# Kernel tuning notes

Measured on AMD Instinct MI355X. Metric: run time of the kernel, lower is better.

## Reference

```python
import jax, jax.numpy as jnp
import numpy as np

SIGMA = 300.0      # args.sigma (temporal gaussian kernel width, frames)
DECAY = 0.9        # args.memory_decay; avg() uses weight = 1/decay per older entry
W_TIME = 1.0       # args.temporal_weight
ORIG_LOSS = 1.0    # args.originalloss_weight
EPS = 1e-7         # BCE clamp


def _get_msg(bank_values, bank_times, bank_mask, ids, times, future):
    """Vectorized MessagePassing.get_msg: per-(id,time) gather of stored
    messages, temporal-kernel + decay weighted average. Mirrors avg():
    out = sum_i dw_i * kernel_i * v_i / sum_i dw_i, dw_i = (1/decay)^rank_i
    with rank over entries passing the past/future condition, zeros if empty."""
    vals = bank_values[ids]                      # [N, M, C]
    ts = bank_times[ids].astype(jnp.float32)     # [N, M]
    mk = bank_mask[ids]                          # [N, M]
    t0 = times.astype(jnp.float32)[:, None]      # [N, 1]
    cond = (ts > t0) if future else (ts < t0)
    m = (mk & cond).astype(vals.dtype)           # [N, M]
    kern = jnp.exp(-((ts - t0) ** 2) / (2.0 * SIGMA ** 2))
    rank = jnp.cumsum(m, axis=1) - m             # exclusive rank among valid entries
    dw = ((1.0 / DECAY) ** rank) * m             # decay weights, masked
    num = jnp.einsum('nm,nmc->nc', dw * kern, vals)
    den = jnp.sum(dw, axis=1, keepdims=True)     # denominator excludes kernel (as avg())
    msg = jnp.where(den > 0, num / jnp.maximum(den, EPS), 0.0)
    return msg * W_TIME


def _bce(p, t):
    p = jnp.clip(p, EPS, 1.0 - EPS)
    return -jnp.mean(t * jnp.log(p) + (1.0 - t) * jnp.log(1.0 - p))


def setup_inputs() -> dict:
    key = jax.random.key(0)
    k = jax.random.split(key, 8)
    N, C, NUM_IDS, M = 512, 157, 10000, 20
    return {
        'a': jax.random.normal(k[0], (N, C), jnp.float32),
        'aa': jax.random.normal(k[1], (N, C, C), jnp.float32),
        'target': jax.random.uniform(k[2], (N, C), jnp.float32),
        'bank_values': jax.random.uniform(k[3], (NUM_IDS, M, C), jnp.float32),
        'bank_times': jax.random.randint(k[4], (NUM_IDS, M), 0, 1000, jnp.int32),
        'bank_mask': jnp.ones((NUM_IDS, M), dtype=bool),
        'ids': jax.random.randint(k[5], (N,), 0, NUM_IDS, jnp.int32),
        'times': jax.random.randint(k[6], (N,), 0, 1000, jnp.int32),
    }


def reference(a, aa, target, bank_values, bank_times, bank_mask, ids, times):
    # msg/fmsg come from stored (detached) data in the original
    msg = jax.lax.stop_gradient(_get_msg(bank_values, bank_times, bank_mask, ids, times, future=False))
    fmsg = jax.lax.stop_gradient(_get_msg(bank_values, bank_times, bank_mask, ids, times, future=True))
    # qa = a + sum_i aa[n,i,j]*msg[n,i] + sum_j aa[n,i,j]*fmsg[n,j]
    qa = a + jnp.einsum('nij,ni->nj', aa, msg) + jnp.einsum('nij,nj->ni', aa, fmsg)
    qa = jax.nn.sigmoid(qa)
    loss = _bce(qa, target) + _bce(jax.nn.sigmoid(a), target) * ORIG_LOSS
    # training, adjustment=False: pastloss = futureloss = 0
    loss = loss / 3.0
    return qa, loss
```

## Files before the change

### kernel.cpp

```cpp
#include <hip/hip_runtime.h>
#include <math.h>

#define N 512
#define C 157
#define M 20

__device__ __forceinline__ float sigmoidf_(float x) {
    return 1.0f / (1.0f + __expf(-x));
}
__device__ __forceinline__ float ntload(const float* p) {
    return __builtin_nontemporal_load(p);
}

__global__ __launch_bounds__(256) void atf_main_kernel(
    const float* __restrict__ a,
    const float* __restrict__ aa,
    const float* __restrict__ target,
    const float* __restrict__ bank_values,
    const int* __restrict__ bank_times,
    const int* __restrict__ bank_mask,
    const int* __restrict__ ids,
    const int* __restrict__ times,
    float* __restrict__ out,
    float* __restrict__ loss_part)
{
    const int n    = blockIdx.x;
    const int tid  = threadIdx.x;
    const int wave = tid >> 6;
    const int lane = tid & 63;

    __shared__ float s_ts[M];
    __shared__ int   s_mk[M];
    __shared__ float s_msg[C];
    __shared__ float s_fmsg[C];
    __shared__ float s_row[C];
    __shared__ float s_colp[4][C];
    __shared__ float s_red[4];

    const int   id = ids[n];
    const float t0 = (float)times[n];

    if (tid < M) {
        s_ts[tid] = (float)bank_times[(size_t)id * M + tid];
        s_mk[tid] = (bank_mask[(size_t)id * M + tid] != 0) ? 1 : 0;
    }
    __syncthreads();

    if (tid < C) {
        const float inv2s2 = 1.0f / (2.0f * 300.0f * 300.0f);
        const float INVDEC = 1.0f / 0.9f;
        float accP = 0.f, accF = 0.f, denP = 0.f, denF = 0.f;
        float wP = 1.f, wF = 1.f;
        const float* vb = bank_values + (size_t)id * M * C + tid;
        #pragma unroll
        for (int m = 0; m < M; ++m) {
            const float ts = s_ts[m];
            const float d  = ts - t0;
            const float kern = __expf(-d * d * inv2s2);
            const float v = vb[m * C];
            const bool mk = (s_mk[m] != 0);
            if (mk && ts < t0) { accP += wP * kern * v; denP += wP; wP *= INVDEC; }
            if (mk && ts > t0) { accF += wF * kern * v; denF += wF; wF *= INVDEC; }
        }
        s_msg[tid]  = (denP > 0.f) ? accP / fmaxf(denP, 1e-7f) : 0.0f;
        s_fmsg[tid] = (denF > 0.f) ? accF / fmaxf(denF, 1e-7f) : 0.0f;
    }
    __syncthreads();

    const float* aan = aa + (size_t)n * C * C;
    const int j0 = lane, j1 = lane + 64, j2 = lane + 128;
    float col0 = 0.f, col1 = 0.f, col2 = 0.f;
    const float f0 = s_fmsg[j0];
    const float f1 = (j1 < C) ? s_fmsg[j1] : 0.0f;
    const float f2 = (j2 < C) ? s_fmsg[j2] : 0.0f;
    const bool ok1 = (j1 < C), ok2 = (j2 < C);

    for (int i = wave; i < C; i += 8) {
        const int ib = i + 4;
        const float* rowA = aan + i * C;
        const float mA = s_msg[i];
        const float a0 = ntload(rowA + j0);
        const float a1 = ok1 ? ntload(rowA + j1) : 0.0f;
        const float a2 = ok2 ? ntload(rowA + j2) : 0.0f;

        float b0 = 0.f, b1 = 0.f, b2 = 0.f, mB = 0.f;
        if (ib < C) {
            const float* rowB = aan + ib * C;
            mB = s_msg[ib];
            b0 = ntload(rowB + j0);
            b1 = ok1 ? ntload(rowB + j1) : 0.0f;
            b2 = ok2 ? ntload(rowB + j2) : 0.0f;
        }

        col0 += a0 * mA + b0 * mB;
        col1 += a1 * mA + b1 * mB;
        col2 += a2 * mA + b2 * mB;

        float rpA = a0 * f0 + a1 * f1 + a2 * f2;
        float rpB = b0 * f0 + b1 * f1 + b2 * f2;
        #pragma unroll
        for (int off = 32; off > 0; off >>= 1) {
            rpA += __shfl_down(rpA, off, 64);
            rpB += __shfl_down(rpB, off, 64);
        }
        if (lane == 0) {
            s_row[i] = rpA;
            if (ib < C) s_row[ib] = rpB;
        }
    }
    s_colp[wave][j0] = col0;
    if (ok1) s_colp[wave][j1] = col1;
    if (ok2) s_colp[wave][j2] = col2;
    __syncthreads();

    float local = 0.0f;
    if (tid < C) {
        const float colsum = s_colp[0][tid] + s_colp[1][tid] + s_colp[2][tid] + s_colp[3][tid];
        const float av = a[(size_t)n * C + tid];
        const float qlin = av + colsum + s_row[tid];
        const float p = sigmoidf_(qlin);
        out[(size_t)n * C + tid] = p;

        const float t = target[(size_t)n * C + tid];
        float pc = fminf(fmaxf(p, 1e-7f), 1.0f - 1e-7f);
        float pa = sigmoidf_(av);
        pa = fminf(fmaxf(pa, 1e-7f), 1.0f - 1e-7f);
        local = t * logf(pc) + (1.0f - t) * logf(1.0f - pc)
              + t * logf(pa) + (1.0f - t) * logf(1.0f - pa);
    }
    #pragma unroll
    for (int off = 32; off > 0; off >>= 1) local += __shfl_down(local, off, 64);
    if (lane == 0) s_red[wave] = local;
    __syncthreads();
    if (tid == 0) {
        loss_part[n] = s_red[0] + s_red[1] + s_red[2] + s_red[3];
    }
}

__global__ __launch_bounds__(256) void atf_finalize_kernel(
    const float* __restrict__ loss_part,
    float* __restrict__ out)
{
    const int tid  = threadIdx.x;
    const int wave = tid >> 6;
    const int lane = tid & 63;
    __shared__ double s_red[4];

    double local = (double)loss_part[tid] + (double)loss_part[tid + 256];
    #pragma unroll
    for (int off = 32; off > 0; off >>= 1) local += __shfl_down(local, off, 64);
    if (lane == 0) s_red[wave] = local;
    __syncthreads();
    if (tid == 0) {
        const double s = s_red[0] + s_red[1] + s_red[2] + s_red[3];
        out[N * C] = (float)(-s / ((double)(N * C) * 3.0));
    }
}

extern "C" void kernel_launch(void* const* d_in, const int* in_sizes, int n_in,
                              void* d_out, int out_size, void* d_ws, size_t ws_size,
                              hipStream_t stream) {
    const float* a           = (const float*)d_in[0];
    const float* aa          = (const float*)d_in[1];
    const float* target      = (const float*)d_in[2];
    const float* bank_values = (const float*)d_in[3];
    const int*   bank_times  = (const int*)d_in[4];
    const int*   bank_mask   = (const int*)d_in[5];
    const int*   ids         = (const int*)d_in[6];
    const int*   times       = (const int*)d_in[7];

    float* out       = (float*)d_out;
    float* loss_part = (float*)d_ws;

    atf_main_kernel<<<N, 256, 0, stream>>>(a, aa, target, bank_values, bank_times,
                                           bank_mask, ids, times, out, loss_part);
    atf_finalize_kernel<<<1, 256, 0, stream>>>(loss_part, out);
}
```

Baseline: 219.0 us.

## Split per-sample einsum into half tiles staged to LDS via async global loads

The fused per-sample kernel is split into an einsum kernel and a separate epilogue kernel. The einsum kernel runs two 512-thread blocks per sample, each covering half of the rows. Each block bulk-copies its slice of aa into shared memory with 16-byte global_load_lds instructions, and the message computation runs while those copies are in flight. Column and row partial sums are then computed from shared memory and written to workspace, where the epilogue combines them with the sigmoid and BCE. This aims to put more memory requests in flight and replace per-row shuffle reductions, at the cost of a large LDS footprint per block, an extra launch and workspace traffic, and 16-byte copies from addresses that are not 16-byte aligned for odd samples.

Result: no change. 215.7 us (-1.5%).

```diff
diff --git a/kernel.cpp b/kernel.cpp
--- a/kernel.cpp
+++ b/kernel.cpp
@@ -4,23 +4,117 @@
 #define N 512
 #define C 157
 #define M 20
+#define RH0 79
+#define TILE_MAX (RH0 * C)
 
 __device__ __forceinline__ float sigmoidf_(float x) {
     return 1.0f / (1.0f + __expf(-x));
 }
-__device__ __forceinline__ float ntload(const float* p) {
-    return __builtin_nontemporal_load(p);
+
+__device__ __forceinline__ void async_cp16(const float* g, float* l) {
+    __builtin_amdgcn_global_load_lds(
+        (const __attribute__((address_space(1))) void*)g,
+        (__attribute__((address_space(3))) void*)l, 16, 0, 0);
 }
 
-__global__ __launch_bounds__(256) void atf_main_kernel(
-    const float* __restrict__ a,
+#define WS_CP 0
+#define WS_RS (N * 2 * C)
+#define WS_LP (WS_RS + N * C)
+
+__global__ __launch_bounds__(512) void atf_einsum_kernel(
     const float* __restrict__ aa,
-    const float* __restrict__ target,
     const float* __restrict__ bank_values,
     const int* __restrict__ bank_times,
     const int* __restrict__ bank_mask,
     const int* __restrict__ ids,
     const int* __restrict__ times,
+    float* __restrict__ ws)
+{
+    const int n   = blockIdx.x >> 1;
+    const int h   = blockIdx.x & 1;
+    const int i0  = h * RH0;
+    const int RH  = h ? (C - RH0) : RH0;
+    const int len = RH * C;
+
+    const int tid  = threadIdx.x;
+    const int wave = tid >> 6;
+    const int lane = tid & 63;
+
+    __shared__ float tile[TILE_MAX];
+    __shared__ float s_msg[C];
+    __shared__ float s_fmsg[C];
+    __shared__ float s_colp[3][C];
+    __shared__ float s_rowp[3][RH0];
+
+    const int   id = ids[n];
+    const float t0 = (float)times[n];
+    const float* aan = aa + (size_t)n * C * C + i0 * C;
+
+    const int full = len >> 8;
+    for (int c = wave; c < full; c += 8) {
+        async_cp16(aan + (c << 8) + lane * 4, &tile[c << 8]);
+    }
+    {
+        const int idx = (full << 8) + tid;
+        if (idx < len) tile[idx] = aan[idx];
+    }
+
+    if (tid < C) {
+        const float inv2s2 = 1.0f / (2.0f * 300.0f * 300.0f);
+        const float INVDEC = 1.0f / 0.9f;
+        float accP = 0.f, accF = 0.f, denP = 0.f, denF = 0.f;
+        float wP = 1.f, wF = 1.f;
+        const float* vb = bank_values + (size_t)id * M * C + tid;
+        const int* tsrow = bank_times + (size_t)id * M;
+        const int* mkrow = bank_mask + (size_t)id * M;
+        #pragma unroll
+        for (int m = 0; m < M; ++m) {
+            const float ts = (float)tsrow[m];
+            const float d  = ts - t0;
+            const float kern = __expf(-d * d * inv2s2);
+            const float v = vb[m * C];
+            const bool mk = (mkrow[m] != 0);
+            if (mk && ts < t0) { accP += wP * kern * v; denP += wP; wP *= INVDEC; }
+            if (mk && ts > t0) { accF += wF * kern * v; denF += wF; wF *= INVDEC; }
+        }
+        s_msg[tid]  = (denP > 0.f) ? accP / fmaxf(denP, 1e-7f) : 0.0f;
+        s_fmsg[tid] = (denF > 0.f) ? accF / fmaxf(denF, 1e-7f) : 0.0f;
+    }
+
+    __syncthreads();
+
+    if (tid < 3 * C) {
+        const int j   = tid % C;
+        const int seg = tid / C;
+        const int r0 = (seg * RH) / 3, r1 = ((seg + 1) * RH) / 3;
+        float acc = 0.f;
+        for (int r = r0; r < r1; ++r) acc += tile[r * C + j] * s_msg[i0 + r];
+        s_colp[seg][j] = acc;
+    }
+    if (tid < 3 * RH) {
+        const int r   = tid % RH;
+        const int seg = tid / RH;
+        const int j0 = (seg * C) / 3, j1 = ((seg + 1) * C) / 3;
+        float acc = 0.f;
+        for (int j = j0; j < j1; ++j) acc += tile[r * C + j] * s_fmsg[j];
+        s_rowp[seg][r] = acc;
+    }
+    __syncthreads();
+
+    if (tid < C) {
+        ws[WS_CP + ((size_t)(2 * n + h)) * C + tid] =
+            s_colp[0][tid] + s_colp[1][tid] + s_colp[2][tid];
+    }
+    if (tid < RH) {
+        ws[WS_RS + (size_t)n * C + i0 + tid] =
+            s_rowp[0][tid] + s_rowp[1][tid] + s_rowp[2][tid];
+    }
+}
+
+__global__ __launch_bounds__(256) void atf_epilogue_kernel(
+    const float* __restrict__ a,
+    const float* __restrict__ target,
+    const float* __restrict__ ws,
     float* __restrict__ out,
     float* __restrict__ loss_part)
 {
@@ -28,96 +122,15 @@
     const int tid  = threadIdx.x;
     const int wave = tid >> 6;
     const int lane = tid & 63;
-
-    __shared__ float s_ts[M];
-    __shared__ int   s_mk[M];
-    __shared__ float s_msg[C];
-    __shared__ float s_fmsg[C];
-    __shared__ float s_row[C];
-    __shared__ float s_colp[4][C];
     __shared__ float s_red[4];
-
-    const int   id = ids[n];
-    const float t0 = (float)times[n];
-
-    if (tid < M) {
-        s_ts[tid] = (float)bank_times[(size_t)id * M + tid];
-        s_mk[tid] = (bank_mask[(size_t)id * M + tid] != 0) ? 1 : 0;
-    }
-    __syncthreads();
-
-    if (tid < C) {
-        const float inv2s2 = 1.0f / (2.0f * 300.0f * 300.0f);
-        const float INVDEC = 1.0f / 0.9f;
-        float accP = 0.f, accF = 0.f, denP = 0.f, denF = 0.f;
-        float wP = 1.f, wF = 1.f;
-        const float* vb = bank_values + (size_t)id * M * C + tid;
-        #pragma unroll
-        for (int m = 0; m < M; ++m) {
-            const float ts = s_ts[m];
-            const float d  = ts - t0;
-            const float kern = __expf(-d * d * inv2s2);
-            const float v = vb[m * C];
-            const bool mk = (s_mk[m] != 0);
-            if (mk && ts < t0) { accP += wP * kern * v; denP += wP; wP *= INVDEC; }
-            if (mk && ts > t0) { accF += wF * kern * v; denF += wF; wF *= INVDEC; }
-        }
-        s_msg[tid]  = (denP > 0.f) ? accP / fmaxf(denP, 1e-7f) : 0.0f;
-        s_fmsg[tid] = (denF > 0.f) ? accF / fmaxf(denF, 1e-7f) : 0.0f;
-    }
-    __syncthreads();
-
-    const float* aan = aa + (size_t)n * C * C;
-    const int j0 = lane, j1 = lane + 64, j2 = lane + 128;
-    float col0 = 0.f, col1 = 0.f, col2 = 0.f;
-    const float f0 = s_fmsg[j0];
-    const float f1 = (j1 < C) ? s_fmsg[j1] : 0.0f;
-    const float f2 = (j2 < C) ? s_fmsg[j2] : 0.0f;
-    const bool ok1 = (j1 < C), ok2 = (j2 < C);
-
-    for (int i = wave; i < C; i += 8) {
-        const int ib = i + 4;
-        const float* rowA = aan + i * C;
-        const float mA = s_msg[i];
-        const float a0 = ntload(rowA + j0);
-        const float a1 = ok1 ? ntload(rowA + j1) : 0.0f;
-        const float a2 = ok2 ? ntload(rowA + j2) : 0.0f;
-
-        float b0 = 0.f, b1 = 0.f, b2 = 0.f, mB = 0.f;
-        if (ib < C) {
-            const float* rowB = aan + ib * C;
-            mB = s_msg[ib];
-            b0 = ntload(rowB + j0);
-            b1 = ok1 ? ntload(rowB + j1) : 0.0f;
-            b2 = ok2 ? ntload(rowB + j2) : 0.0f;
-        }
-
-        col0 += a0 * mA + b0 * mB;
-        col1 += a1 * mA + b1 * mB;
-        col2 += a2 * mA + b2 * mB;
-
-        float rpA = a0 * f0 + a1 * f1 + a2 * f2;
-        float rpB = b0 * f0 + b1 * f1 + b2 * f2;
-        #pragma unroll
-        for (int off = 32; off > 0; off >>= 1) {
-            rpA += __shfl_down(rpA, off, 64);
-            rpB += __shfl_down(rpB, off, 64);
-        }
-        if (lane == 0) {
-            s_row[i] = rpA;
-            if (ib < C) s_row[ib] = rpB;
-        }
-    }
-    s_colp[wave][j0] = col0;
-    if (ok1) s_colp[wave][j1] = col1;
-    if (ok2) s_colp[wave][j2] = col2;
-    __syncthreads();
 
     float local = 0.0f;
     if (tid < C) {
-        const float colsum = s_colp[0][tid] + s_colp[1][tid] + s_colp[2][tid] + s_colp[3][tid];
+        const float colsum = ws[WS_CP + ((size_t)(2 * n)) * C + tid]
+                           + ws[WS_CP + ((size_t)(2 * n + 1)) * C + tid];
+        const float rowsum = ws[WS_RS + (size_t)n * C + tid];
         const float av = a[(size_t)n * C + tid];
-        const float qlin = av + colsum + s_row[tid];
+        const float qlin = av + colsum + rowsum;
         const float p = sigmoidf_(qlin);
         out[(size_t)n * C + tid] = p;
 
@@ -132,9 +145,7 @@
     for (int off = 32; off > 0; off >>= 1) local += __shfl_down(local, off, 64);
     if (lane == 0) s_red[wave] = local;
     __syncthreads();
-    if (tid == 0) {
-        loss_part[n] = s_red[0] + s_red[1] + s_red[2] + s_red[3];
-    }
+    if (tid == 0) loss_part[n] = s_red[0] + s_red[1] + s_red[2] + s_red[3];
 }
 
 __global__ __launch_bounds__(256) void atf_finalize_kernel(
@@ -169,10 +180,11 @@
     const int*   ids         = (const int*)d_in[6];
     const int*   times       = (const int*)d_in[7];
 
-    float* out       = (float*)d_out;
-    float* loss_part = (float*)d_ws;
+    float* out = (float*)d_out;
+    float* ws  = (float*)d_ws;
 
-    atf_main_kernel<<<N, 256, 0, stream>>>(a, aa, target, bank_values, bank_times,
-                                           bank_mask, ids, times, out, loss_part);
-    atf_finalize_kernel<<<1, 256, 0, stream>>>(loss_part, out);
+    atf_einsum_kernel<<<N * 2, 512, 0, stream>>>(aa, bank_values, bank_times,
+                                                 bank_mask, ids, times, ws);
+    atf_epilogue_kernel<<<N, 256, 0, stream>>>(a, target, ws, out, ws + WS_LP);
+    atf_finalize_kernel<<<1, 256, 0, stream>>>(ws + WS_LP, out);
 }
```
